# Performance work log

Hardware: AMD Instinct MI355X
Metric: run time of the kernel (lower is better)

The kernel has to match this reference:

```python
import jax, jax.numpy as jnp
import numpy as np

B, C, H, W, D, V = 1, 32, 128, 160, 48, 3


def _make_proj_matrices():
    # K @ [R|t] per view, small rotations/baselines so warps land mostly in-bounds
    K = np.array([[400.0, 0.0, 80.0], [0.0, 400.0, 64.0], [0.0, 0.0, 1.0]])
    mats = []
    for v in range(V):
        a = 0.04 * v
        R = np.array([[np.cos(a), 0.0, np.sin(a)], [0.0, 1.0, 0.0], [-np.sin(a), 0.0, np.cos(a)]])
        t = np.array([120.0 * v, 0.0, 0.0])  # baseline in mm, consistent with depth ~425..935
        P = np.eye(4)
        P[:3, :3] = K @ R
        P[:3, 3] = K @ t
        mats.append(P)
    return jnp.asarray(np.stack(mats)[None], dtype=jnp.float32)  # [1,V,4,4]


def setup_inputs() -> dict:
    key = jax.random.key(0)
    k0, k1, k2, kw = jax.random.split(key, 4)
    feat0 = jax.random.normal(k0, (B, C, H, W), jnp.float32)
    feat1 = jax.random.normal(k1, (B, C, H, W), jnp.float32)
    feat2 = jax.random.normal(k2, (B, C, H, W), jnp.float32)
    depth_values = jnp.broadcast_to(
        jnp.linspace(425.0, 935.0, D, dtype=jnp.float32)[None], (B, D))
    w_reg = jax.random.normal(kw, (1, C, 3, 3, 3), jnp.float32) * 0.05
    b_reg = jnp.zeros((1,), jnp.float32)
    return dict(feat0=feat0, feat1=feat1, feat2=feat2,
                proj_matrices=_make_proj_matrices(),
                depth_values=depth_values, w_reg=w_reg, b_reg=b_reg,
                num_depth=D)


def _bilinear_sample(fea, gx, gy):
    # fea: [C,H,W]; gx,gy: [N] pixel coords (align_corners=True convention),
    # zero padding outside image (matches F.grid_sample padding_mode='zeros').
    h, w = fea.shape[1], fea.shape[2]
    x0 = jnp.floor(gx)
    y0 = jnp.floor(gy)
    wx = gx - x0
    wy = gy - y0

    def corner(xi, yi, wgt):
        valid = ((xi >= 0) & (xi <= w - 1) & (yi >= 0) & (yi <= h - 1)).astype(fea.dtype)
        xc = jnp.clip(xi, 0, w - 1).astype(jnp.int32)
        yc = jnp.clip(yi, 0, h - 1).astype(jnp.int32)
        return fea[:, yc, xc] * (wgt * valid)[None]  # [C,N]

    return (corner(x0, y0, (1 - wx) * (1 - wy)) +
            corner(x0 + 1, y0, wx * (1 - wy)) +
            corner(x0, y0 + 1, (1 - wx) * wy) +
            corner(x0 + 1, y0 + 1, wx * wy))


def homo_warping(src_fea, src_proj, ref_proj, depth_values):
    # src_fea [B,C,H,W], projs [B,4,4], depth_values [B,D] -> [B,C,D,H,W]
    b, c, h, w = src_fea.shape
    d = depth_values.shape[1]
    proj = src_proj @ jnp.linalg.inv(ref_proj)
    rot = proj[:, :3, :3]           # [B,3,3]
    trans = proj[:, :3, 3]          # [B,3]
    yy, xx = jnp.meshgrid(jnp.arange(h, dtype=src_fea.dtype),
                          jnp.arange(w, dtype=src_fea.dtype), indexing='ij')
    xyz = jnp.stack([xx.ravel(), yy.ravel(), jnp.ones(h * w, src_fea.dtype)], 0)  # [3,HW]
    rot_xyz = jnp.einsum('bij,jn->bin', rot, xyz)                                  # [B,3,HW]
    p = rot_xyz[:, :, None, :] * depth_values[:, None, :, None] + trans[:, :, None, None]  # [B,3,D,HW]
    z = p[:, 2]
    gx = (p[:, 0] / z).reshape(b, -1)  # [B, D*HW]
    gy = (p[:, 1] / z).reshape(b, -1)
    warped = jax.vmap(_bilinear_sample)(src_fea, gx, gy)  # [B,C,D*HW]
    return warped.reshape(b, c, d, h, w)


def reference(feat0, feat1, feat2, proj_matrices, depth_values, w_reg, b_reg, num_depth):
    features = [feat0, feat1, feat2]
    projs = [proj_matrices[:, v] for v in range(proj_matrices.shape[1])]
    ref_fea, ref_proj = features[0], projs[0]
    num_views = len(features)
    b, c, h, w = ref_fea.shape

    ref_volume = jnp.broadcast_to(ref_fea[:, :, None], (b, c, num_depth, h, w))
    volume_sum = ref_volume
    volume_sq_sum = ref_volume ** 2
    for src_fea, src_proj in zip(features[1:], projs[1:]):
        wv = homo_warping(src_fea, src_proj, ref_proj, depth_values)
        volume_sum = volume_sum + wv
        volume_sq_sum = volume_sq_sum + wv * wv

    volume_variance = volume_sq_sum / num_views - (volume_sum / num_views) ** 2

    # cost_regularization stand-in: 3D conv C -> 1, SAME padding, then squeeze channel
    cost = jax.lax.conv_general_dilated(
        volume_variance, w_reg, window_strides=(1, 1, 1), padding='SAME',
        dimension_numbers=('NCDHW', 'OIDHW', 'NCDHW'))
    cost = cost[:, 0] + b_reg[0]            # [B,D,H,W]

    prob_volume = jax.nn.softmax(cost, axis=1)
    depth = jnp.sum(prob_volume * depth_values[:, :, None, None], axis=1)  # [B,H,W]
    photometric_confidence = jnp.max(prob_volume, axis=1)                   # [B,H,W]
    return depth, photometric_confidence
```

## Files before the change

kernel.cpp:

```cpp
#include <hip/hip_runtime.h>
#include <hip/hip_fp16.h>
#include <math.h>

#define Cc 32
#define Hc 128
#define Wc 160
#define Dc 48
#define HWc (Hc*Wc)
#define TS 16
#define HALO (TS+2)
#define NPOS (HALO*HALO)
#define DCHUNK 8
#define NCHUNK (Dc/DCHUNK)
#define NPASS 6
#define NSLOT (DCHUNK+2)


typedef _Float16 h8v __attribute__((ext_vector_type(8)));
typedef float f32x4 __attribute__((ext_vector_type(4)));

union F4H { float4 f; __half2 h[4]; };
union PackCW { __half2 h[4]; float4 f; };
union AF { float4 f; h8v h; };

__global__ void k_pre(const float* __restrict__ f0, const float* __restrict__ f1,
                      const float* __restrict__ f2, const float* __restrict__ proj,
                      const float* __restrict__ wreg,
                      _Float16* __restrict__ o0, _Float16* __restrict__ o1, _Float16* __restrict__ o2,
                      float* __restrict__ wsproj, _Float16* __restrict__ w2h,
                      float* __restrict__ costvol) {
    const int tid = threadIdx.x;
    const int p = blockIdx.x * 256 + tid;
    if (blockIdx.y == 3) {
        if (p < HWc) {
#pragma unroll
            for (int d = 0; d < Dc; d++) costvol[d * HWc + p] = 0.f;
        }
        return;
    }
    if (p < HWc) {
        const float* f = (blockIdx.y == 0) ? f0 : (blockIdx.y == 1) ? f1 : f2;
        _Float16*    o = (blockIdx.y == 0) ? o0 : (blockIdx.y == 1) ? o1 : o2;
        float v[Cc];
#pragma unroll
        for (int c = 0; c < Cc; c++) v[c] = f[c * HWc + p];
        union { __half2 h[16]; float4 f4[4]; } rec;
#pragma unroll
        for (int c = 0; c < 16; c++) rec.h[c] = __floats2half2_rn(v[2 * c], v[2 * c + 1]);
        float4* o4 = (float4*)(o + (size_t)p * Cc);
#pragma unroll
        for (int j = 0; j < 4; j++) o4[j] = rec.f4[j];
    }
    if (blockIdx.x == 0 && blockIdx.y == 0) {
        for (int i = tid; i < 9 * 3 * Cc; i += 256) {
            int ch = i & 31;
            int t  = i >> 5;
            int kd = t % 3;
            int khkw = t / 3;
            w2h[i] = (_Float16)wreg[ch * 27 + kd * 9 + khkw];
        }
        if (tid == 0) {
            float a[4][8];
            for (int i = 0; i < 4; i++)
                for (int j = 0; j < 4; j++) {
                    a[i][j]     = proj[i * 4 + j];
                    a[i][j + 4] = (i == j) ? 1.f : 0.f;
                }
            for (int col = 0; col < 4; col++) {
                int piv = col; float best = fabsf(a[col][col]);
                for (int r = col + 1; r < 4; r++) {
                    float v = fabsf(a[r][col]);
                    if (v > best) { best = v; piv = r; }
                }
                if (piv != col)
                    for (int j = 0; j < 8; j++) { float t = a[col][j]; a[col][j] = a[piv][j]; a[piv][j] = t; }
                float inv = 1.f / a[col][col];
                for (int j = 0; j < 8; j++) a[col][j] *= inv;
                for (int r = 0; r < 4; r++) if (r != col) {
                    float f = a[r][col];
                    for (int j = 0; j < 8; j++) a[r][j] -= f * a[col][j];
                }
            }
            for (int v = 1; v < 3; v++) {
                const float* P = proj + v * 16;
                float M[3][4];
                for (int i = 0; i < 3; i++)
                    for (int j = 0; j < 4; j++) {
                        float s = 0.f;
                        for (int k = 0; k < 4; k++) s += P[i * 4 + k] * a[k][4 + j];
                        M[i][j] = s;
                    }
                float* o = wsproj + (v - 1) * 12;
                o[0] = M[0][0]; o[1] = M[0][1]; o[2] = M[0][2];
                o[3] = M[1][0]; o[4] = M[1][1]; o[5] = M[1][2];
                o[6] = M[2][0]; o[7] = M[2][1]; o[8] = M[2][2];
                o[9] = M[0][3]; o[10] = M[1][3]; o[11] = M[2][3];
            }
        }
    }
}

__global__ __launch_bounds__(256, 2) void k_cost(
    const _Float16* __restrict__ fT0, const _Float16* __restrict__ fT1,
    const _Float16* __restrict__ fT2, const float* __restrict__ dvals,
    const float4* __restrict__ w2h4, const float* __restrict__ wsproj,
    float* __restrict__ costvol)
{
    __shared__ float4 varA[NPOS * 4];
    __shared__ float4 varB[NPOS * 4];
    __shared__ float4 parW[NPOS];
    __shared__ float4 parI[NPOS];
    __shared__ float4 cost_l4[NSLOT * 64];
    __shared__ float projl[24];
    float* cost_l = (float*)cost_l4;

    const int tid = threadIdx.x;
    if (tid < 24) projl[tid] = wsproj[tid];
#pragma unroll
    for (int i = 0; i < NSLOT; i++) cost_l[i * 256 + tid] = 0.f;
    __syncthreads();

    const int tileX = blockIdx.x;
    const int tileY = blockIdx.y;
    const int d0    = blockIdx.z * DCHUNK;
    const int baseH = tileY * TS - 1, baseW = tileX * TS - 1;

    const int posq = tid >> 2;
    const int cc   = tid & 3;

    const int wid  = tid >> 6;
    const int lane = tid & 63;
    const int lrow = lane & 15;
    const int lsel = lane >> 4;

    const float4* fT0_4 = (const float4*)fT0;
    const float4* fT1_4 = (const float4*)fT1;
    const float4* fT2_4 = (const float4*)fT2;

    h8v bfr[9];
    {
        const int kdc = (lrow < 3) ? lrow : 0;
#pragma unroll
        for (int t = 0; t < 9; t++) {
            AF u; u.f = w2h4[(t * 3 + kdc) * 4 + lsel];
            bfr[t] = u.h;
        }
    }

    float rAx[2][2], rAy[2][2], rAz[2][2];
    float trn[2][3];
#pragma unroll
    for (int v = 0; v < 2; v++) {
        trn[v][0] = projl[v * 12 + 9];
        trn[v][1] = projl[v * 12 + 10];
        trn[v][2] = projl[v * 12 + 11];
    }
    int amask = 0;
#pragma unroll
    for (int s = 0; s < 2; s++) {
        int p = tid + s * 256;
        bool act = p < NPOS;
        int pp = act ? p : 0;
        int py = pp / HALO, px = pp % HALO;
        int hyi = baseH + py, hxi = baseW + px;
        bool ok = act && hyi >= 0 && hyi < Hc && hxi >= 0 && hxi < Wc;
        if (ok) amask |= (1 << s);
        float hx = (float)hxi, hy = (float)hyi;
#pragma unroll
        for (int v = 0; v < 2; v++) {
            const float* R = projl + v * 12;
            rAx[s][v] = fmaf(R[0], hx, fmaf(R[1], hy, R[2]));
            rAy[s][v] = fmaf(R[3], hx, fmaf(R[4], hy, R[5]));
            rAz[s][v] = fmaf(R[6], hx, fmaf(R[7], hy, R[8]));
        }
    }

    int    bmask = 0;
    float4 rfv[NPASS];
#pragma unroll
    for (int s = 0; s < NPASS; s++) {
        int p = posq + s * 64;
        bool act = p < NPOS;
        int pp = act ? p : 0;
        int py = pp / HALO, px = pp % HALO;
        int hyi = baseH + py, hxi = baseW + px;
        bool ok = act && hyi >= 0 && hyi < Hc && hxi >= 0 && hxi < Wc;
        if (ok) bmask |= (1 << s);
        rfv[s] = ok ? fT0_4[(hyi * Wc + hxi) * 4 + cc] : make_float4(0.f, 0.f, 0.f, 0.f);
    }

    auto phaseA = [&](int dpn) {
        const float depthN = dvals[dpn];
#pragma unroll
        for (int s = 0; s < 2; s++) {
            int p = tid + s * 256;
            if (p >= NPOS) break;
            if (!((amask >> s) & 1)) continue;
            float cw[2][4]; unsigned int pk[4];
#pragma unroll
            for (int v = 0; v < 2; v++) {
                float X = fmaf(rAx[s][v], depthN, trn[v][0]);
                float Y = fmaf(rAy[s][v], depthN, trn[v][1]);
                float Z = fmaf(rAz[s][v], depthN, trn[v][2]);
                float iz = 1.f / Z;
                float gx = X * iz, gy = Y * iz;
                float x0f = floorf(gx), y0f = floorf(gy);
                float wx = gx - x0f, wy = gy - y0f;
                int x0 = (int)x0f, y0 = (int)y0f;
                bool vx0 = (x0 >= 0) & (x0 <= Wc - 1);
                bool vx1 = (x0 + 1 >= 0) & (x0 + 1 <= Wc - 1);
                bool vy0 = (y0 >= 0) & (y0 <= Hc - 1);
                bool vy1 = (y0 + 1 >= 0) & (y0 + 1 <= Hc - 1);
                int xc0 = min(max(x0, 0), Wc - 1), xc1 = min(max(x0 + 1, 0), Wc - 1);
                int yc0 = min(max(y0, 0), Hc - 1), yc1 = min(max(y0 + 1, 0), Hc - 1);
                float ax = 1.f - wx, ay = 1.f - wy;
                cw[v][0] = (vx0 && vy0) ? ax * ay : 0.f;
                cw[v][1] = (vx1 && vy0) ? wx * ay : 0.f;
                cw[v][2] = (vx0 && vy1) ? ax * wy : 0.f;
                cw[v][3] = (vx1 && vy1) ? wx * wy : 0.f;
                unsigned int i0 = (unsigned int)(yc0 * Wc + xc0);
                unsigned int i1 = (unsigned int)(yc0 * Wc + xc1);
                unsigned int i2 = (unsigned int)(yc1 * Wc + xc0);
                unsigned int i3 = (unsigned int)(yc1 * Wc + xc1);
                pk[v * 2 + 0] = i0 | (i1 << 16);
                pk[v * 2 + 1] = i2 | (i3 << 16);
            }
            PackCW pc;
            pc.h[0] = __floats2half2_rn(cw[0][0], cw[0][1]);
            pc.h[1] = __floats2half2_rn(cw[0][2], cw[0][3]);
            pc.h[2] = __floats2half2_rn(cw[1][0], cw[1][1]);
            pc.h[3] = __floats2half2_rn(cw[1][2], cw[1][3]);
            parW[p] = pc.f;
            parI[p] = make_float4(__uint_as_float(pk[0]), __uint_as_float(pk[1]),
                                  __uint_as_float(pk[2]), __uint_as_float(pk[3]));
        }
    };

    const __half2 kT3 = __float2half2_rn(1.f / 3.f);
    const __half2 kN9 = __float2half2_rn(-1.f / 9.f);

    auto phaseB = [&](float4* dst) {
#pragma unroll
        for (int s = 0; s < NPASS; s++) {
            int p = posq + s * 64;
            if (p >= NPOS) continue;
            const int vaddr = (p << 2) + (cc ^ ((p >> 1) & 3));
            if (!((bmask >> s) & 1)) {
                dst[vaddr] = make_float4(0.f, 0.f, 0.f, 0.f);
                continue;
            }
            PackCW pc; pc.f = parW[p];
            float4 pkf = parI[p];
            __half2 c0a = __low2half2(pc.h[0]), c0b = __high2half2(pc.h[0]);
            __half2 c0c = __low2half2(pc.h[1]), c0d = __high2half2(pc.h[1]);
            __half2 c1a = __low2half2(pc.h[2]), c1b = __high2half2(pc.h[2]);
            __half2 c1c = __low2half2(pc.h[3]), c1d = __high2half2(pc.h[3]);
            unsigned int u0 = __float_as_uint(pkf.x), u1 = __float_as_uint(pkf.y);
            unsigned int u2 = __float_as_uint(pkf.z), u3 = __float_as_uint(pkf.w);
            int i00 = u0 & 0xffff, i01 = u0 >> 16, i02 = u1 & 0xffff, i03 = u1 >> 16;
            int i10 = u2 & 0xffff, i11 = u2 >> 16, i12 = u3 & 0xffff, i13 = u3 >> 16;
            F4H rf; rf.f = rfv[s];
            F4H t00, t01, t10, t11, u00v, u01v, u10v, u11v, vo;
            t00.f = fT1_4[i00 * 4 + cc];
            t01.f = fT1_4[i01 * 4 + cc];
            t10.f = fT1_4[i02 * 4 + cc];
            t11.f = fT1_4[i03 * 4 + cc];
            u00v.f = fT2_4[i10 * 4 + cc];
            u01v.f = fT2_4[i11 * 4 + cc];
            u10v.f = fT2_4[i12 * 4 + cc];
            u11v.f = fT2_4[i13 * 4 + cc];
#pragma unroll
            for (int j = 0; j < 4; j++) {
                __half2 a1 = __hfma2(c0a, t00.h[j], __hfma2(c0b, t01.h[j],
                             __hfma2(c0c, t10.h[j], __hmul2(c0d, t11.h[j]))));
                __half2 a2 = __hfma2(c1a, u00v.h[j], __hfma2(c1b, u01v.h[j],
                             __hfma2(c1c, u10v.h[j], __hmul2(c1d, u11v.h[j]))));
                __half2 r  = rf.h[j];
                __half2 sm = __hadd2(r, __hadd2(a1, a2));
                __half2 sq = __hfma2(r, r, __hfma2(a1, a1, __hmul2(a2, a2)));
                vo.h[j] = __hfma2(__hmul2(sm, sm), kN9, __hmul2(sq, kT3));
            }
            dst[vaddr] = vo.f;
        }
    };

    auto conv = [&](const float4* src, int dp) {
#pragma unroll
        for (int g = 0; g < 4; g++) {
            const int R = (wid << 2) + g;
            f32x4 acc = {0.f, 0.f, 0.f, 0.f};
#pragma unroll
            for (int t = 0; t < 9; t++) {
                const int dy = t / 3, dx = t % 3;
                const int pos = (R + dy) * HALO + dx + lrow;
                AF a; a.f = src[(pos << 2) + (lsel ^ ((pos >> 1) & 3))];
                acc = __builtin_amdgcn_mfma_f32_16x16x32_f16(a.h, bfr[t], acc, 0, 0, 0);
            }
            if (lrow < 3) {
                const int idx = ((dp - d0) + 2 - lrow) * 64 + R * 4 + lsel;
                float4 c = cost_l4[idx];
                c.x += acc[0]; c.y += acc[1]; c.z += acc[2]; c.w += acc[3];
                cost_l4[idx] = c;
            }
        }
    };

    const int dpLast = d0 + DCHUNK - 1;

    phaseA(d0);
    __syncthreads();
    phaseB(varA);
    __syncthreads();
    phaseA(d0 + 1);
    __syncthreads();

    for (int i = 0; i < DCHUNK / 2; i++) {
        const int t = d0 + 2 * i;
        phaseB(varB);
        conv(varA, t);
        __syncthreads();
        if (t + 2 <= dpLast) {
            phaseA(t + 2);
            __syncthreads();
        }
        if (t + 2 <= dpLast) phaseB(varA);
        conv(varB, t + 1);
        __syncthreads();
        if (t + 3 <= dpLast) {
            phaseA(t + 3);
            __syncthreads();
        }
    }

    const int gy = tileY * TS + (tid >> 4), gx = tileX * TS + (tid & 15);
    float* cbase = costvol + gy * Wc + gx;
#pragma unroll
    for (int slot = 0; slot < NSLOT; slot++) {
        const int s = d0 + slot - 1;
        if (s >= 0 && s < Dc)
            atomicAdd(cbase + (size_t)s * HWc, cost_l[slot * 256 + tid]);
    }
}

__global__ void k_softmax(const float* __restrict__ costvol, const float* __restrict__ dvals,
                          const float* __restrict__ breg, float* __restrict__ out)
{
    const int px = blockIdx.x * 256 + threadIdx.x;
    if (px >= HWc) return;
    const float bias = breg[0];
    float c[Dc];
    float m = -1e30f;
#pragma unroll
    for (int d = 0; d < Dc; d++) {
        c[d] = costvol[d * HWc + px] + bias;
        m = fmaxf(m, c[d]);
    }
    float se = 0.f, sed = 0.f, me = 0.f;
#pragma unroll
    for (int d = 0; d < Dc; d++) {
        float e = __expf(c[d] - m);
        se += e;
        sed = fmaf(e, dvals[d], sed);
        me = fmaxf(me, e);
    }
    float inv = 1.f / se;
    out[px]       = sed * inv;
    out[HWc + px] = me * inv;
}

extern "C" void kernel_launch(void* const* d_in, const int* in_sizes, int n_in,
                              void* d_out, int out_size, void* d_ws, size_t ws_size,
                              hipStream_t stream) {
    const float* f0    = (const float*)d_in[0];
    const float* f1    = (const float*)d_in[1];
    const float* f2    = (const float*)d_in[2];
    const float* proj  = (const float*)d_in[3];
    const float* dvals = (const float*)d_in[4];
    const float* wreg  = (const float*)d_in[5];
    const float* breg  = (const float*)d_in[6];

    float* ws      = (float*)d_ws;
    float* wsproj  = ws;
    _Float16* w2h  = (_Float16*)(ws + 32);
    _Float16* fT0h = (_Float16*)(ws + 32 + 432);
    _Float16* fT1h = fT0h + (size_t)HWc * Cc;
    _Float16* fT2h = fT1h + (size_t)HWc * Cc;
    float* costvol = (float*)(fT2h + (size_t)HWc * Cc);

    k_pre<<<dim3((HWc + 255) / 256, 4), 256, 0, stream>>>(f0, f1, f2, proj, wreg,
                                                          fT0h, fT1h, fT2h, wsproj, w2h,
                                                          costvol);

    dim3 grid(Wc / TS, Hc / TS, NCHUNK);
    k_cost<<<grid, 256, 0, stream>>>(fT0h, fT1h, fT2h, dvals, (const float4*)w2h,
                                     wsproj, costvol);

    k_softmax<<<(HWc + 255) / 256, 256, 0, stream>>>(costvol, dvals, breg, (float*)d_out);
}
```

Measured before the change: 123.3 us.

## Halve k_cost tile height to 16x8 and raise occupancy to 4 blocks/CU

Shrinks the spatial tile of the cost kernel from 16x16 to 16x8 so the halo fits in one thread per position for the warp-parameter phase. This halves the per-block shared memory, doubles the grid, and raises the launch bound to four blocks per CU. The cost is a larger halo fraction, which means more redundant warp computation and feature loads per output pixel. Each block also does more atomic flushes of its cost slots relative to the useful work it produces.

```diff
diff --git a/kernel.cpp b/kernel.cpp
--- a/kernel.cpp
+++ b/kernel.cpp
@@ -7,12 +7,14 @@
 #define Wc 160
 #define Dc 48
 #define HWc (Hc*Wc)
-#define TS 16
-#define HALO (TS+2)
-#define NPOS (HALO*HALO)
+#define TSX 16
+#define TSY 8
+#define HALOX (TSX+2)
+#define HALOY (TSY+2)
+#define NPOS (HALOX*HALOY)
 #define DCHUNK 8
 #define NCHUNK (Dc/DCHUNK)
-#define NPASS 6
+#define NPASS 3
 #define NSLOT (DCHUNK+2)
 
 
@@ -100,7 +102,7 @@
     }
 }
 
-__global__ __launch_bounds__(256, 2) void k_cost(
+__global__ __launch_bounds__(256, 4) void k_cost(
     const _Float16* __restrict__ fT0, const _Float16* __restrict__ fT1,
     const _Float16* __restrict__ fT2, const float* __restrict__ dvals,
     const float4* __restrict__ w2h4, const float* __restrict__ wsproj,
@@ -110,20 +112,20 @@
     __shared__ float4 varB[NPOS * 4];
     __shared__ float4 parW[NPOS];
     __shared__ float4 parI[NPOS];
-    __shared__ float4 cost_l4[NSLOT * 64];
+    __shared__ float4 cost_l4[NSLOT * 32];
     __shared__ float projl[24];
     float* cost_l = (float*)cost_l4;
 
     const int tid = threadIdx.x;
     if (tid < 24) projl[tid] = wsproj[tid];
 #pragma unroll
-    for (int i = 0; i < NSLOT; i++) cost_l[i * 256 + tid] = 0.f;
+    for (int i = 0; i < 5; i++) cost_l[i * 256 + tid] = 0.f;
     __syncthreads();
 
     const int tileX = blockIdx.x;
-    const int tileY = blockIdx.y;
+    const int sy    = blockIdx.y;
     const int d0    = blockIdx.z * DCHUNK;
-    const int baseH = tileY * TS - 1, baseW = tileX * TS - 1;
+    const int baseH = sy * TSY - 1, baseW = tileX * TSX - 1;
 
     const int posq = tid >> 2;
     const int cc   = tid & 3;
@@ -147,7 +149,7 @@
         }
     }
 
-    float rAx[2][2], rAy[2][2], rAz[2][2];
+    float rAx[2], rAy[2], rAz[2];
     float trn[2][3];
 #pragma unroll
     for (int v = 0; v < 2; v++) {
@@ -155,23 +157,19 @@
         trn[v][1] = projl[v * 12 + 10];
         trn[v][2] = projl[v * 12 + 11];
     }
-    int amask = 0;
-#pragma unroll
-    for (int s = 0; s < 2; s++) {
-        int p = tid + s * 256;
-        bool act = p < NPOS;
-        int pp = act ? p : 0;
-        int py = pp / HALO, px = pp % HALO;
+    bool aok;
+    {
+        int pp = (tid < NPOS) ? tid : 0;
+        int py = pp / HALOX, px = pp % HALOX;
         int hyi = baseH + py, hxi = baseW + px;
-        bool ok = act && hyi >= 0 && hyi < Hc && hxi >= 0 && hxi < Wc;
-        if (ok) amask |= (1 << s);
+        aok = (tid < NPOS) && hyi >= 0 && hyi < Hc && hxi >= 0 && hxi < Wc;
         float hx = (float)hxi, hy = (float)hyi;
 #pragma unroll
         for (int v = 0; v < 2; v++) {
             const float* R = projl + v * 12;
-            rAx[s][v] = fmaf(R[0], hx, fmaf(R[1], hy, R[2]));
-            rAy[s][v] = fmaf(R[3], hx, fmaf(R[4], hy, R[5]));
-            rAz[s][v] = fmaf(R[6], hx, fmaf(R[7], hy, R[8]));
+            rAx[v] = fmaf(R[0], hx, fmaf(R[1], hy, R[2]));
+            rAy[v] = fmaf(R[3], hx, fmaf(R[4], hy, R[5]));
+            rAz[v] = fmaf(R[6], hx, fmaf(R[7], hy, R[8]));
         }
     }
 
@@ -182,7 +180,7 @@
         int p = posq + s * 64;
         bool act = p < NPOS;
         int pp = act ? p : 0;
-        int py = pp / HALO, px = pp % HALO;
+        int py = pp / HALOX, px = pp % HALOX;
         int hyi = baseH + py, hxi = baseW + px;
         bool ok = act && hyi >= 0 && hyi < Hc && hxi >= 0 && hxi < Wc;
         if (ok) bmask |= (1 << s);
@@ -191,17 +189,13 @@
 
     auto phaseA = [&](int dpn) {
         const float depthN = dvals[dpn];
-#pragma unroll
-        for (int s = 0; s < 2; s++) {
-            int p = tid + s * 256;
-            if (p >= NPOS) break;
-            if (!((amask >> s) & 1)) continue;
+        if (aok) {
             float cw[2][4]; unsigned int pk[4];
 #pragma unroll
             for (int v = 0; v < 2; v++) {
-                float X = fmaf(rAx[s][v], depthN, trn[v][0]);
-                float Y = fmaf(rAy[s][v], depthN, trn[v][1]);
-                float Z = fmaf(rAz[s][v], depthN, trn[v][2]);
+                float X = fmaf(rAx[v], depthN, trn[v][0]);
+                float Y = fmaf(rAy[v], depthN, trn[v][1]);
+                float Z = fmaf(rAz[v], depthN, trn[v][2]);
                 float iz = 1.f / Z;
                 float gx = X * iz, gy = Y * iz;
                 float x0f = floorf(gx), y0f = floorf(gy);
@@ -230,9 +224,9 @@
             pc.h[1] = __floats2half2_rn(cw[0][2], cw[0][3]);
             pc.h[2] = __floats2half2_rn(cw[1][0], cw[1][1]);
             pc.h[3] = __floats2half2_rn(cw[1][2], cw[1][3]);
-            parW[p] = pc.f;
-            parI[p] = make_float4(__uint_as_float(pk[0]), __uint_as_float(pk[1]),
-                                  __uint_as_float(pk[2]), __uint_as_float(pk[3]));
+            parW[tid] = pc.f;
+            parI[tid] = make_float4(__uint_as_float(pk[0]), __uint_as_float(pk[1]),
+                                    __uint_as_float(pk[2]), __uint_as_float(pk[3]));
         }
     };
 
@@ -286,18 +280,18 @@
 
     auto conv = [&](const float4* src, int dp) {
 #pragma unroll
-        for (int g = 0; g < 4; g++) {
-            const int R = (wid << 2) + g;
+        for (int g = 0; g < 2; g++) {
+            const int R = (wid << 1) + g;
             f32x4 acc = {0.f, 0.f, 0.f, 0.f};
 #pragma unroll
             for (int t = 0; t < 9; t++) {
                 const int dy = t / 3, dx = t % 3;
-                const int pos = (R + dy) * HALO + dx + lrow;
+                const int pos = (R + dy) * HALOX + dx + lrow;
                 AF a; a.f = src[(pos << 2) + (lsel ^ ((pos >> 1) & 3))];
                 acc = __builtin_amdgcn_mfma_f32_16x16x32_f16(a.h, bfr[t], acc, 0, 0, 0);
             }
             if (lrow < 3) {
-                const int idx = ((dp - d0) + 2 - lrow) * 64 + R * 4 + lsel;
+                const int idx = ((dp - d0) + 2 - lrow) * 32 + R * 4 + lsel;
                 float4 c = cost_l4[idx];
                 c.x += acc[0]; c.y += acc[1]; c.z += acc[2]; c.w += acc[3];
                 cost_l4[idx] = c;
@@ -332,13 +326,16 @@
         }
     }
 
-    const int gy = tileY * TS + (tid >> 4), gx = tileX * TS + (tid & 15);
+    const int c    = tid & 127;
+    const int half = tid >> 7;
+    const int gy = sy * TSY + (c >> 4), gx = tileX * TSX + (c & 15);
     float* cbase = costvol + gy * Wc + gx;
 #pragma unroll
-    for (int slot = 0; slot < NSLOT; slot++) {
+    for (int k = 0; k < 5; k++) {
+        const int slot = half * 5 + k;
         const int s = d0 + slot - 1;
         if (s >= 0 && s < Dc)
-            atomicAdd(cbase + (size_t)s * HWc, cost_l[slot * 256 + tid]);
+            atomicAdd(cbase + (size_t)s * HWc, cost_l[slot * 128 + c]);
     }
 }
 
@@ -391,7 +388,7 @@
                                                           fT0h, fT1h, fT2h, wsproj, w2h,
                                                           costvol);
 
-    dim3 grid(Wc / TS, Hc / TS, NCHUNK);
+    dim3 grid(Wc / TSX, Hc / TSY, NCHUNK);
     k_cost<<<grid, 256, 0, stream>>>(fT0h, fT1h, fT2h, dvals, (const float4*)w2h,
                                      wsproj, costvol);
 
```

New measurement: 118.4 us. 4.0% less time.
